# Kernel optimization log

Measured on AMD Instinct MI355X. Metric: run time of the kernel, lower is better.

The kernel has to match this reference:

```python
import jax, jax.numpy as jnp
import numpy as np

EPS = 1e-10

def setup_inputs() -> dict:
    key = jax.random.key(0)
    k1, k2, k3 = jax.random.split(key, 3)
    B, R, S, C = 4, 4096, 96, 32
    colors = jax.random.uniform(k1, (B, R, S, C), dtype=jnp.float32)
    densities = jax.random.normal(k2, (B, R, S, 1), dtype=jnp.float32)
    # depths: sorted increasing along the sample axis, in a plausible near/far range
    depths = jnp.sort(jax.random.uniform(k3, (B, R, S, 1), dtype=jnp.float32) * 1.8 + 0.8, axis=2)
    return {"colors": colors, "densities": densities, "depths": depths}

def reference(colors, densities, depths):
    # clamp_mode == 'softplus', white_back == False, foreground-only path
    deltas = depths[:, :, 1:] - depths[:, :, :-1]                      # [B,R,S-1,1]
    colors_mid = (colors[:, :, :-1] + colors[:, :, 1:]) * 0.5          # [B,R,S-1,C]
    densities_mid = (densities[:, :, :-1] + densities[:, :, 1:]) * 0.5
    depths_mid = (depths[:, :, :-1] + depths[:, :, 1:]) * 0.5

    densities_mid = jax.nn.softplus(densities_mid - 1.0)
    density_delta = densities_mid * deltas
    alpha = 1.0 - jnp.exp(-density_delta)                              # [B,R,S-1,1]

    ones = jnp.ones_like(alpha[:, :, :1])
    alpha_shifted = jnp.concatenate([ones, 1.0 - alpha + EPS], axis=-2)  # [B,R,S,1]
    transmittance = jnp.cumprod(alpha_shifted, axis=-2)                # per-ray scan
    weights = alpha * transmittance[:, :, :-1]                         # [B,R,S-1,1]
    weight_bg = transmittance[:, :, -1][..., None]                     # [B,R,1,1]

    composite_rgb = jnp.sum(weights * colors_mid, axis=-2)             # [B,R,C]
    weight_total = jnp.sum(weights, axis=2)                            # [B,R,1]
    composite_depth = jnp.sum(weights * depths_mid, axis=-2) / weight_total
    composite_depth = jnp.where(jnp.isnan(composite_depth), jnp.inf, composite_depth)
    composite_depth = jnp.clip(composite_depth, jnp.min(depths), jnp.max(depths))

    composite_rgb = composite_rgb * 2.0 - 1.0
    return composite_rgb, composite_depth, weights, alpha, weight_bg
```

## Files before the change

kernel.cpp:

```cpp
#include <hip/hip_runtime.h>
#include <math.h>

#define NS 96
#define SM1 95
#define NC 32
#define REPS 1e-10f

__global__ __launch_bounds__(256) void raymarch_main(
    const float* __restrict__ colors,
    const float* __restrict__ densities,
    const float* __restrict__ depths,
    float* __restrict__ out_rgb,
    float* __restrict__ out_depth,
    float* __restrict__ out_w,
    float* __restrict__ out_alpha,
    float* __restrict__ out_wbg,
    float* __restrict__ ws_d0,
    float* __restrict__ ws_d1)
{
    const int ray = blockIdx.x;
    const int tid = threadIdx.x;

    __shared__ float s_dep[NS];
    __shared__ float s_den[NS];
    __shared__ float s_alpha[SM1];
    __shared__ float s_oma[SM1];
    __shared__ float s_w[SM1];
    __shared__ float s_coeff[NS];
    __shared__ float s_red[256 * 4];

    const float4* col4 = (const float4*)(colors + (size_t)ray * NS * NC);
    float4 v0 = col4[tid];
    float4 v1 = col4[256 + tid];
    float4 v2 = col4[512 + tid];

    const float* dep = depths + (size_t)ray * NS;
    const float* den = densities + (size_t)ray * NS;

    if (tid < NS) {
        s_dep[tid] = dep[tid];
        s_den[tid] = den[tid];
    }
    __syncthreads();

    if (tid < SM1) {
        float dm = 0.5f * (s_den[tid] + s_den[tid + 1]) - 1.0f;
        float sp = fmaxf(dm, 0.0f) + log1pf(expf(-fabsf(dm)));
        float dd = sp * (s_dep[tid + 1] - s_dep[tid]);
        float a = 1.0f - expf(-dd);
        s_alpha[tid] = a;
        s_oma[tid] = 1.0f - a + REPS;
        out_alpha[(size_t)ray * SM1 + tid] = a;
    }
    __syncthreads();

    if (tid == 0) {
        float T = 1.0f, wsum = 0.0f, dsum = 0.0f;
        #pragma unroll 5
        for (int i = 0; i < SM1; ++i) {
            float w = s_alpha[i] * T;
            s_w[i] = w;
            wsum += w;
            dsum += w * (0.5f * (s_dep[i] + s_dep[i + 1]));
            T *= s_oma[i];
        }
        out_wbg[ray] = T;
        float cd = dsum / wsum;
        if (cd != cd) cd = __builtin_inff();
        out_depth[ray] = cd;
        ws_d0[ray] = s_dep[0];
        ws_d1[ray] = s_dep[NS - 1];
    }
    __syncthreads();

    if (tid < NS) {
        float wprev = (tid >= 1)  ? s_w[tid - 1] : 0.0f;
        float wcur  = (tid < SM1) ? s_w[tid]     : 0.0f;
        s_coeff[tid] = 0.5f * (wprev + wcur);
    }
    if (tid < SM1) {
        out_w[(size_t)ray * SM1 + tid] = s_w[tid];
    }
    __syncthreads();

    float4 acc;
    {
        float c0 = s_coeff[tid >> 3];
        float c1 = s_coeff[(256 + tid) >> 3];
        float c2 = s_coeff[(512 + tid) >> 3];
        acc.x = fmaf(c0, v0.x, fmaf(c1, v1.x, c2 * v2.x));
        acc.y = fmaf(c0, v0.y, fmaf(c1, v1.y, c2 * v2.y));
        acc.z = fmaf(c0, v0.z, fmaf(c1, v1.z, c2 * v2.z));
        acc.w = fmaf(c0, v0.w, fmaf(c1, v1.w, c2 * v2.w));
    }
    s_red[tid * 4 + 0] = acc.x;
    s_red[tid * 4 + 1] = acc.y;
    s_red[tid * 4 + 2] = acc.z;
    s_red[tid * 4 + 3] = acc.w;
    __syncthreads();

    if (tid < NC) {
        float sum = 0.0f;
        #pragma unroll
        for (int m = 0; m < 32; ++m) {
            sum += s_red[m * 32 + tid];
        }
        out_rgb[(size_t)ray * NC + tid] = 2.0f * sum - 1.0f;
    }
}

__global__ __launch_bounds__(256) void raymarch_finalize(
    const float* __restrict__ ws_d0,
    const float* __restrict__ ws_d1,
    float* __restrict__ out_depth,
    int rays)
{
    __shared__ float s_mn[256];
    __shared__ float s_mx[256];
    const int tid = threadIdx.x;

    float mn = __builtin_inff();
    float mx = -__builtin_inff();
    for (int r = tid; r < rays; r += 256) {
        mn = fminf(mn, ws_d0[r]);
        mx = fmaxf(mx, ws_d1[r]);
    }
    s_mn[tid] = mn;
    s_mx[tid] = mx;
    __syncthreads();
    for (int off = 128; off > 0; off >>= 1) {
        if (tid < off) {
            s_mn[tid] = fminf(s_mn[tid], s_mn[tid + off]);
            s_mx[tid] = fmaxf(s_mx[tid], s_mx[tid + off]);
        }
        __syncthreads();
    }
    const float dmin = s_mn[0];
    const float dmax = s_mx[0];

    const int r = blockIdx.x * 256 + tid;
    if (r < rays) {
        float cd = out_depth[r];
        cd = fminf(fmaxf(cd, dmin), dmax);
        out_depth[r] = cd;
    }
}

extern "C" void kernel_launch(void* const* d_in, const int* in_sizes, int n_in,
                              void* d_out, int out_size, void* d_ws, size_t ws_size,
                              hipStream_t stream) {
    const float* colors    = (const float*)d_in[0];
    const float* densities = (const float*)d_in[1];
    const float* depths    = (const float*)d_in[2];

    const int rays = in_sizes[2] / NS;

    float* out = (float*)d_out;
    float* out_rgb   = out;
    float* out_depth = out_rgb + (size_t)rays * NC;
    float* out_w     = out_depth + rays;
    float* out_alpha = out_w + (size_t)rays * SM1;
    float* out_wbg   = out_alpha + (size_t)rays * SM1;

    float* ws    = (float*)d_ws;
    float* ws_d0 = ws;
    float* ws_d1 = ws + rays;

    raymarch_main<<<rays, 256, 0, stream>>>(
        colors, densities, depths,
        out_rgb, out_depth, out_w, out_alpha, out_wbg, ws_d0, ws_d1);

    raymarch_finalize<<<(rays + 255) / 256, 256, 0, stream>>>(
        ws_d0, ws_d1, out_depth, rays);
}
```

Before: 305.4 us.

## Split ray kernel into parallel-scan and color-composite kernels

Replaces the single-thread serial transmittance loop with a Hillis-Steele parallel product scan and tree reductions for weight and depth sums, running in a separate 128-thread kernel. Color compositing moves into its own kernel, which reads per-sample coefficients back from workspace. This is meant to remove the serial 95-step bottleneck that stalls each block while color loads sit in registers. In exchange it adds an extra launch and a global round-trip for the coefficients, and the scan's product order differs from the serial cumprod.

```diff
diff --git a/kernel.cpp b/kernel.cpp
--- a/kernel.cpp
+++ b/kernel.cpp
@@ -6,106 +6,133 @@
 #define NC 32
 #define REPS 1e-10f
 
-__global__ __launch_bounds__(256) void raymarch_main(
-    const float* __restrict__ colors,
+__global__ __launch_bounds__(128) void raymarch_scan(
     const float* __restrict__ densities,
     const float* __restrict__ depths,
-    float* __restrict__ out_rgb,
     float* __restrict__ out_depth,
     float* __restrict__ out_w,
     float* __restrict__ out_alpha,
     float* __restrict__ out_wbg,
+    float* __restrict__ ws_coeff,
     float* __restrict__ ws_d0,
     float* __restrict__ ws_d1)
 {
     const int ray = blockIdx.x;
-    const int tid = threadIdx.x;
+    const int t = threadIdx.x;
 
     __shared__ float s_dep[NS];
     __shared__ float s_den[NS];
     __shared__ float s_alpha[SM1];
-    __shared__ float s_oma[SM1];
+    __shared__ float s_scan[SM1];
     __shared__ float s_w[SM1];
-    __shared__ float s_coeff[NS];
-    __shared__ float s_red[256 * 4];
-
-    const float4* col4 = (const float4*)(colors + (size_t)ray * NS * NC);
-    float4 v0 = col4[tid];
-    float4 v1 = col4[256 + tid];
-    float4 v2 = col4[512 + tid];
+    __shared__ float s_a[128];
+    __shared__ float s_b[128];
 
     const float* dep = depths + (size_t)ray * NS;
     const float* den = densities + (size_t)ray * NS;
 
-    if (tid < NS) {
-        s_dep[tid] = dep[tid];
-        s_den[tid] = den[tid];
-    }
-    __syncthreads();
-
-    if (tid < SM1) {
-        float dm = 0.5f * (s_den[tid] + s_den[tid + 1]) - 1.0f;
+    if (t < NS) {
+        s_dep[t] = dep[t];
+        s_den[t] = den[t];
+    }
+    __syncthreads();
+
+    if (t < SM1) {
+        float dm = 0.5f * (s_den[t] + s_den[t + 1]) - 1.0f;
         float sp = fmaxf(dm, 0.0f) + log1pf(expf(-fabsf(dm)));
-        float dd = sp * (s_dep[tid + 1] - s_dep[tid]);
+        float dd = sp * (s_dep[t + 1] - s_dep[t]);
         float a = 1.0f - expf(-dd);
-        s_alpha[tid] = a;
-        s_oma[tid] = 1.0f - a + REPS;
-        out_alpha[(size_t)ray * SM1 + tid] = a;
-    }
-    __syncthreads();
-
-    if (tid == 0) {
-        float T = 1.0f, wsum = 0.0f, dsum = 0.0f;
-        #pragma unroll 5
-        for (int i = 0; i < SM1; ++i) {
-            float w = s_alpha[i] * T;
-            s_w[i] = w;
-            wsum += w;
-            dsum += w * (0.5f * (s_dep[i] + s_dep[i + 1]));
-            T *= s_oma[i];
+        s_alpha[t] = a;
+        s_scan[t] = 1.0f - a + REPS;
+        out_alpha[(size_t)ray * SM1 + t] = a;
+    }
+    __syncthreads();
+
+    #pragma unroll
+    for (int off = 1; off < SM1; off <<= 1) {
+        float x = 1.0f;
+        if (t >= off && t < SM1) x = s_scan[t - off];
+        __syncthreads();
+        if (t >= off && t < SM1) s_scan[t] *= x;
+        __syncthreads();
+    }
+
+    float w = 0.0f;
+    if (t < SM1) {
+        float T = (t == 0) ? 1.0f : s_scan[t - 1];
+        w = s_alpha[t] * T;
+        s_w[t] = w;
+        out_w[(size_t)ray * SM1 + t] = w;
+    }
+    s_a[t] = w;
+    s_b[t] = (t < SM1) ? w * 0.5f * (s_dep[t] + s_dep[t + 1]) : 0.0f;
+    __syncthreads();
+
+    #pragma unroll
+    for (int off = 64; off > 0; off >>= 1) {
+        if (t < off) {
+            s_a[t] += s_a[t + off];
+            s_b[t] += s_b[t + off];
         }
-        out_wbg[ray] = T;
-        float cd = dsum / wsum;
+        __syncthreads();
+    }
+
+    if (t == 0) {
+        out_wbg[ray] = s_scan[SM1 - 1];
+        float cd = s_b[0] / s_a[0];
         if (cd != cd) cd = __builtin_inff();
         out_depth[ray] = cd;
         ws_d0[ray] = s_dep[0];
         ws_d1[ray] = s_dep[NS - 1];
     }
-    __syncthreads();
-
-    if (tid < NS) {
-        float wprev = (tid >= 1)  ? s_w[tid - 1] : 0.0f;
-        float wcur  = (tid < SM1) ? s_w[tid]     : 0.0f;
-        s_coeff[tid] = 0.5f * (wprev + wcur);
-    }
-    if (tid < SM1) {
-        out_w[(size_t)ray * SM1 + tid] = s_w[tid];
-    }
-    __syncthreads();
-
+    if (t < NS) {
+        float wprev = (t >= 1)  ? s_w[t - 1] : 0.0f;
+        float wcur  = (t < SM1) ? s_w[t]     : 0.0f;
+        ws_coeff[(size_t)ray * NS + t] = 0.5f * (wprev + wcur);
+    }
+}
+
+__global__ __launch_bounds__(256) void raymarch_color(
+    const float* __restrict__ colors,
+    const float* __restrict__ ws_coeff,
+    float* __restrict__ out_rgb)
+{
+    const int ray = blockIdx.x;
+    const int t = threadIdx.x;
+
+    __shared__ float s_coeff[NS];
+    __shared__ float s_red[256 * 4];
+
+    const float4* col4 = (const float4*)(colors + (size_t)ray * NS * NC);
+    float4 v0 = col4[t];
+    float4 v1 = col4[256 + t];
+    float4 v2 = col4[512 + t];
+
+    if (t < NS) s_coeff[t] = ws_coeff[(size_t)ray * NS + t];
+    __syncthreads();
+
+    float c0 = s_coeff[t >> 3];
+    float c1 = s_coeff[(256 + t) >> 3];
+    float c2 = s_coeff[(512 + t) >> 3];
     float4 acc;
-    {
-        float c0 = s_coeff[tid >> 3];
-        float c1 = s_coeff[(256 + tid) >> 3];
-        float c2 = s_coeff[(512 + tid) >> 3];
-        acc.x = fmaf(c0, v0.x, fmaf(c1, v1.x, c2 * v2.x));
-        acc.y = fmaf(c0, v0.y, fmaf(c1, v1.y, c2 * v2.y));
-        acc.z = fmaf(c0, v0.z, fmaf(c1, v1.z, c2 * v2.z));
-        acc.w = fmaf(c0, v0.w, fmaf(c1, v1.w, c2 * v2.w));
-    }
-    s_red[tid * 4 + 0] = acc.x;
-    s_red[tid * 4 + 1] = acc.y;
-    s_red[tid * 4 + 2] = acc.z;
-    s_red[tid * 4 + 3] = acc.w;
-    __syncthreads();
-
-    if (tid < NC) {
+    acc.x = fmaf(c0, v0.x, fmaf(c1, v1.x, c2 * v2.x));
+    acc.y = fmaf(c0, v0.y, fmaf(c1, v1.y, c2 * v2.y));
+    acc.z = fmaf(c0, v0.z, fmaf(c1, v1.z, c2 * v2.z));
+    acc.w = fmaf(c0, v0.w, fmaf(c1, v1.w, c2 * v2.w));
+
+    s_red[t * 4 + 0] = acc.x;
+    s_red[t * 4 + 1] = acc.y;
+    s_red[t * 4 + 2] = acc.z;
+    s_red[t * 4 + 3] = acc.w;
+    __syncthreads();
+
+    if (t < NC) {
         float sum = 0.0f;
         #pragma unroll
         for (int m = 0; m < 32; ++m) {
-            sum += s_red[m * 32 + tid];
+            sum += s_red[m * 32 + t];
         }
-        out_rgb[(size_t)ray * NC + tid] = 2.0f * sum - 1.0f;
+        out_rgb[(size_t)ray * NC + t] = 2.0f * sum - 1.0f;
     }
 }
 
@@ -162,13 +189,16 @@
     float* out_alpha = out_w + (size_t)rays * SM1;
     float* out_wbg   = out_alpha + (size_t)rays * SM1;
 
-    float* ws    = (float*)d_ws;
-    float* ws_d0 = ws;
-    float* ws_d1 = ws + rays;
-
-    raymarch_main<<<rays, 256, 0, stream>>>(
-        colors, densities, depths,
-        out_rgb, out_depth, out_w, out_alpha, out_wbg, ws_d0, ws_d1);
+    float* ws       = (float*)d_ws;
+    float* ws_d0    = ws;
+    float* ws_d1    = ws + rays;
+    float* ws_coeff = ws + 2 * (size_t)rays;
+
+    raymarch_scan<<<rays, 128, 0, stream>>>(
+        densities, depths,
+        out_depth, out_w, out_alpha, out_wbg, ws_coeff, ws_d0, ws_d1);
+
+    raymarch_color<<<rays, 256, 0, stream>>>(colors, ws_coeff, out_rgb);
 
     raymarch_finalize<<<(rays + 255) / 256, 256, 0, stream>>>(
         ws_d0, ws_d1, out_depth, rays);
```

Result: slower. 314.7 us (+3.1%).
